# Kernel tuning notes

Hardware: AMD Instinct MI355X
Metric: run time of the kernel (lower is better)

## Reference

```python
import jax, jax.numpy as jnp
import numpy as np

V, D = 1_000_000, 128
N0, N1, N2 = 1_048_576, 131_072, 16_384
E0, E1, EP = 1_048_576, 131_072, 16_384


def setup_inputs() -> dict:
    key = jax.random.key(0)
    ks = jax.random.split(key, 20)
    inp = {
        'emb': jax.random.normal(ks[0], (V, D), jnp.float32) * 0.1,
        'bias': jnp.zeros((V, 1), jnp.float32),
        'nids': jax.random.randint(ks[1], (N0,), 0, V),
        'src0': jax.random.randint(ks[2], (E0,), 0, N0),
        'dst0': jax.random.randint(ks[3], (E0,), 0, N1),
        'w0': jax.random.uniform(ks[4], (E0,), jnp.float32),
        'src1': jax.random.randint(ks[5], (E1,), 0, N1),
        'dst1': jax.random.randint(ks[6], (E1,), 0, N2),
        'w1': jax.random.uniform(ks[7], (E1,), jnp.float32),
        'pos_src': jax.random.randint(ks[8], (EP,), 0, N2),
        'pos_dst': jax.random.randint(ks[9], (EP,), 0, N2),
        'neg_src': jax.random.randint(ks[10], (EP,), 0, N2),
        'neg_dst': jax.random.randint(ks[11], (EP,), 0, N2),
        'Q0w': jax.random.normal(ks[12], (D, D), jnp.float32) / np.sqrt(D),
        'Q0b': jnp.zeros((D,), jnp.float32),
        'W0w': jax.random.normal(ks[13], (2 * D, D), jnp.float32) / np.sqrt(2 * D),
        'W0b': jnp.zeros((D,), jnp.float32),
        'Q1w': jax.random.normal(ks[14], (D, D), jnp.float32) / np.sqrt(D),
        'Q1b': jnp.zeros((D,), jnp.float32),
        'W1w': jax.random.normal(ks[15], (2 * D, D), jnp.float32) / np.sqrt(2 * D),
        'W1b': jnp.zeros((D,), jnp.float32),
    }
    return inp


def _sage_conv(h_src, h_dst, src, dst, w, Qw, Qb, Ww, Wb, n_dst):
    # n = relu(Q h_src); m = sum_e w_e * n[src_e] per dst; ws = sum_e w_e per dst
    n = jax.nn.relu(h_src @ Qw + Qb)                                   # [N_src, H]
    m = jax.ops.segment_sum(n[src] * w[:, None], dst, num_segments=n_dst)
    ws = jnp.clip(jax.ops.segment_sum(w, dst, num_segments=n_dst), 1.0, None)[:, None]
    z = jax.nn.relu(jnp.concatenate([m / ws, h_dst], axis=1) @ Ww + Wb)
    zn = jnp.linalg.norm(z, axis=1, keepdims=True)
    return z / jnp.where(zn == 0, 1.0, zn)


def _pair_score(h, bias_nid, src, dst):
    # u_dot_v + bias_src + bias_dst  -> [E, 1]
    s = jnp.sum(h[src] * h[dst], axis=1, keepdims=True)
    return s + bias_nid[src] + bias_nid[dst]


def reference(emb, bias, nids, src0, dst0, w0, src1, dst1, w1,
              pos_src, pos_dst, neg_src, neg_dst,
              Q0w, Q0b, W0w, W0b, Q1w, Q1b, W1w, W1b):
    h = emb[nids]                                                      # [N0, D]
    h1 = _sage_conv(h, h[:N1], src0, dst0, w0, Q0w, Q0b, W0w, W0b, N1)  # [N1, D]
    h2 = _sage_conv(h1, h1[:N2], src1, dst1, w1, Q1w, Q1b, W1w, W1b, N2)  # [N2, D]
    h_item = emb[nids[:N2]] + h2                                       # [N2, D]
    bias_nid = bias[nids[:N2]]                                         # [N2, 1]
    pos = _pair_score(h_item, bias_nid, pos_src, pos_dst)
    neg = _pair_score(h_item, bias_nid, neg_src, neg_dst)
    return jax.nn.relu(neg - pos + 1.0)                                # [EP, 1]
```

## Files before the change

kernel.cpp:

```cpp
#include <hip/hip_runtime.h>
#include <stdint.h>

#define V_SZ   1000000
#define N0_SZ  1048576
#define N1_SZ  131072
#define N2_SZ  16384
#define E0_SZ  1048576
#define E1_SZ  131072
#define EP_SZ  16384

typedef short bf16x8 __attribute__((ext_vector_type(8)));
typedef float f32x4  __attribute__((ext_vector_type(4)));

__device__ __forceinline__ unsigned short f2bf(float f) {
  union { float f; unsigned u; } v; v.f = f;
  unsigned r = v.u + 0x7FFFu + ((v.u >> 16) & 1u);
  return (unsigned short)(r >> 16);
}
__device__ __forceinline__ float bf2f(unsigned short h) {
  union { unsigned u; float f; } v; v.u = ((unsigned)h) << 16;
  return v.f;
}
__device__ __forceinline__ unsigned pack2bf(float a, float b) {
  return ((unsigned)f2bf(b) << 16) | (unsigned)f2bf(a);
}

__global__ __launch_bounds__(256) void prepw_all_k(
    const float* __restrict__ Q0w, const float* __restrict__ W0w,
    const float* __restrict__ Q1w, const float* __restrict__ W1w,
    unsigned short* __restrict__ Q0T, unsigned short* __restrict__ W0T,
    unsigned short* __restrict__ Q1T, unsigned short* __restrict__ W1T) {
  int t = blockIdx.x * 256 + threadIdx.x;
  const float* W; unsigned short* WT; int K; int base;
  if (t < 16384)      { W = Q0w; WT = Q0T; K = 128; base = 0; }
  else if (t < 49152) { W = W0w; WT = W0T; K = 256; base = 16384; }
  else if (t < 65536) { W = Q1w; WT = Q1T; K = 128; base = 49152; }
  else                { W = W1w; WT = W1T; K = 256; base = 65536; }
  int u = t - base;
  int n = u & 127, k = u >> 7;
  WT[(size_t)n * K + k] = f2bf(W[u]);
}

__global__ __launch_bounds__(256) void hist_all_k(const int* __restrict__ dst0,
                                                  const int* __restrict__ dst1,
                                                  int* __restrict__ counts) {
  int e = blockIdx.x * 256 + threadIdx.x;
  if (e < E0_SZ) atomicAdd(&counts[dst0[e]], 1);
  else if (e < E0_SZ + E1_SZ) atomicAdd(&counts[N1_SZ + dst1[e - E0_SZ]], 1);
}

__global__ __launch_bounds__(256) void scan_bsums_k(const int* __restrict__ counts,
                                                    int* __restrict__ bsums) {
  __shared__ int red[256];
  int base = blockIdx.x * 1024, t = threadIdx.x;
  int s = 0;
  #pragma unroll
  for (int i = 0; i < 4; i++) s += counts[base + t * 4 + i];
  red[t] = s;
  __syncthreads();
  for (int st = 128; st > 0; st >>= 1) {
    if (t < st) red[t] += red[t + st];
    __syncthreads();
  }
  if (t == 0) bsums[blockIdx.x] = red[0];
}

__global__ __launch_bounds__(256) void scan_top2_k(int* __restrict__ bsums,
                                                   int* __restrict__ offs0_last,
                                                   int* __restrict__ offs1_last) {
  __shared__ int lds[256];
  int b = blockIdx.x, t = threadIdx.x;
  int nb = (b == 0) ? 128 : 16;
  int off = (b == 0) ? 0 : 128;
  int v = (t < nb) ? bsums[off + t] : 0;
  lds[t] = v;
  __syncthreads();
  for (int st = 1; st < 256; st <<= 1) {
    int x = (t >= st) ? lds[t - st] : 0;
    __syncthreads();
    lds[t] += x;
    __syncthreads();
  }
  if (t < nb) bsums[off + t] = lds[t] - v;
  if (t == nb - 1) *((b == 0) ? offs0_last : offs1_last) = lds[t];
}

__global__ __launch_bounds__(256) void scan_final_k(const int* __restrict__ counts,
                                                    const int* __restrict__ bsums,
                                                    int* __restrict__ offs0,
                                                    int* __restrict__ offs1) {
  __shared__ int tsum[256];
  int b = blockIdx.x, t = threadIdx.x;
  int base = b * 1024;
  int v0 = counts[base + t * 4 + 0], v1 = counts[base + t * 4 + 1];
  int v2 = counts[base + t * 4 + 2], v3 = counts[base + t * 4 + 3];
  int s = v0 + v1 + v2 + v3;
  tsum[t] = s;
  __syncthreads();
  for (int st = 1; st < 256; st <<= 1) {
    int x = (t >= st) ? tsum[t - st] : 0;
    __syncthreads();
    tsum[t] += x;
    __syncthreads();
  }
  int pre = bsums[b] + tsum[t] - s;
  int* op = (b < 128) ? (offs0 + base) : (offs1 + base - N1_SZ);
  op[t * 4 + 0] = pre;
  op[t * 4 + 1] = pre + v0;
  op[t * 4 + 2] = pre + v0 + v1;
  op[t * 4 + 3] = pre + v0 + v1 + v2;
}

__global__ __launch_bounds__(256) void scatter_all_k(
    const int* __restrict__ src0, const int* __restrict__ dst0, const float* __restrict__ w0,
    const int* __restrict__ src1, const int* __restrict__ dst1, const float* __restrict__ w1,
    const int* __restrict__ offs0, const int* __restrict__ offs1,
    int* __restrict__ cursor,
    int* __restrict__ srcs_s0, float* __restrict__ ws_s0,
    int* __restrict__ srcs_s1, float* __restrict__ ws_s1) {
  int e = blockIdx.x * 256 + threadIdx.x;
  if (e < E0_SZ) {
    int d = dst0[e];
    int p = offs0[d] + atomicAdd(&cursor[d], 1);
    srcs_s0[p] = src0[e];
    ws_s0[p] = w0[e];
  } else if (e < E0_SZ + E1_SZ) {
    int ee = e - E0_SZ;
    int d = dst1[ee];
    int p = offs1[d] + atomicAdd(&cursor[N1_SZ + d], 1);
    srcs_s1[p] = src1[ee];
    ws_s1[p] = w1[ee];
  }
}

#define AM_GATHER 0
#define AM_BF16   1
#define EPI_BF16        0
#define EPI_NORM        1
#define EPI_NORM_ADDEMB 2

template <int KCHUNKS, int AM0, int AM1, int EPI>
__global__ __launch_bounds__(256) void gemm_k(const void* __restrict__ asrc0,
                                              const void* __restrict__ asrc1,
                                              const int* __restrict__ ids,
                                              const unsigned short* __restrict__ BT,
                                              const float* __restrict__ biasv,
                                              void* __restrict__ outp,
                                              const float* __restrict__ emb) {
  __shared__ unsigned short lA[64][136];
  __shared__ unsigned short lB[128][136];
  const int tid = threadIdx.x;
  const int lane = tid & 63;
  const int wid = tid >> 6;
  const int rowbase = blockIdx.x * 64;
  const int Ktot = KCHUNKS * 128;

  f32x4 acc[8];
  #pragma unroll
  for (int i = 0; i < 8; i++) acc[i] = (f32x4){0.f, 0.f, 0.f, 0.f};

  for (int c = 0; c < KCHUNKS; ++c) {
    if (c) __syncthreads();
    const int am = (c == 0) ? AM0 : AM1;
    const void* asrc = (c == 0) ? asrc0 : asrc1;
    if (am == AM_GATHER) {
      const float* fsrc = (const float*)asrc;
      #pragma unroll
      for (int i = 0; i < 8; i++) {
        int f = i * 256 + tid;
        int r = f >> 5, c4 = f & 31;
        const float* rp = fsrc + (size_t)ids[rowbase + r] * 128;
        float4 v = *(const float4*)(rp + c4 * 4);
        uint2 pk;
        pk.x = pack2bf(v.x, v.y);
        pk.y = pack2bf(v.z, v.w);
        *(uint2*)(&lA[r][c4 * 4]) = pk;
      }
    } else {
      const unsigned short* bsrc = (const unsigned short*)asrc;
      #pragma unroll
      for (int i = 0; i < 4; i++) {
        int f = i * 256 + tid;
        int r = f >> 4, c8 = f & 15;
        uint4 v = *(const uint4*)(bsrc + (size_t)(rowbase + r) * 128 + c8 * 8);
        *(uint4*)(&lA[r][c8 * 8]) = v;
      }
    }
    {
      const unsigned short* bp = BT + c * 128;
      #pragma unroll
      for (int i = 0; i < 8; i++) {
        int f = i * 256 + tid;
        int n = f >> 4, c8 = f & 15;
        uint4 v = *(const uint4*)(bp + (size_t)n * Ktot + c8 * 8);
        *(uint4*)(&lB[n][c8 * 8]) = v;
      }
    }
    __syncthreads();

    const int mr = wid * 16 + (lane & 15);
    const int kq = (lane >> 4) * 8;
    #pragma unroll
    for (int kk = 0; kk < 128; kk += 32) {
      bf16x8 af = *(const bf16x8*)(&lA[mr][kk + kq]);
      #pragma unroll
      for (int nt = 0; nt < 8; ++nt) {
        bf16x8 bfr = *(const bf16x8*)(&lB[nt * 16 + (lane & 15)][kk + kq]);
        acc[nt] = __builtin_amdgcn_mfma_f32_16x16x32_bf16(af, bfr, acc[nt], 0, 0, 0);
      }
    }
  }

  const int crow = wid * 16 + ((lane >> 4) << 2);
  float vreg[8][4];
  #pragma unroll
  for (int nt = 0; nt < 8; ++nt) {
    int col = nt * 16 + (lane & 15);
    float b = biasv[col];
    #pragma unroll
    for (int r = 0; r < 4; ++r) {
      float v = acc[nt][r] + b;
      vreg[nt][r] = v > 0.f ? v : 0.f;
    }
  }
  if (EPI == EPI_BF16) {
    unsigned short* op = (unsigned short*)outp;
    #pragma unroll
    for (int nt = 0; nt < 8; ++nt) {
      int col = nt * 16 + (lane & 15);
      #pragma unroll
      for (int r = 0; r < 4; ++r)
        op[(size_t)(rowbase + crow + r) * 128 + col] = f2bf(vreg[nt][r]);
    }
  } else {
    float ss[4] = {0.f, 0.f, 0.f, 0.f};
    #pragma unroll
    for (int nt = 0; nt < 8; ++nt)
      #pragma unroll
      for (int r = 0; r < 4; ++r) ss[r] += vreg[nt][r] * vreg[nt][r];
    #pragma unroll
    for (int r = 0; r < 4; ++r) {
      ss[r] += __shfl_xor(ss[r], 1);
      ss[r] += __shfl_xor(ss[r], 2);
      ss[r] += __shfl_xor(ss[r], 4);
      ss[r] += __shfl_xor(ss[r], 8);
    }
    float sc[4];
    #pragma unroll
    for (int r = 0; r < 4; ++r) sc[r] = ss[r] > 0.f ? rsqrtf(ss[r]) : 1.0f;
    if (EPI == EPI_NORM) {
      unsigned short* op = (unsigned short*)outp;
      #pragma unroll
      for (int nt = 0; nt < 8; ++nt) {
        int col = nt * 16 + (lane & 15);
        #pragma unroll
        for (int r = 0; r < 4; ++r)
          op[(size_t)(rowbase + crow + r) * 128 + col] = f2bf(vreg[nt][r] * sc[r]);
      }
    } else {
      float* op = (float*)outp;
      #pragma unroll
      for (int nt = 0; nt < 8; ++nt) {
        int col = nt * 16 + (lane & 15);
        #pragma unroll
        for (int r = 0; r < 4; ++r) {
          int row = rowbase + crow + r;
          op[(size_t)row * 128 + col] =
              vreg[nt][r] * sc[r] + emb[(size_t)ids[row] * 128 + col];
        }
      }
    }
  }
}

__global__ __launch_bounds__(256) void agg_k(const unsigned short* __restrict__ nsrc,
                                             const int* __restrict__ offs,
                                             const int* __restrict__ srcs_s,
                                             const float* __restrict__ ws_s,
                                             unsigned short* __restrict__ aout, int ndst) {
  int wid = threadIdx.x >> 6, lane = threadIdx.x & 63;
  int d = blockIdx.x * 4 + wid;
  if (d >= ndst) return;
  int beg = offs[d], end = offs[d + 1];
  float ax = 0.f, ay = 0.f, wsum = 0.f;
  for (int base = beg; base < end; base += 64) {
    int cnt = min(64, end - base);
    int sv = 0; float wv = 0.f;
    if (lane < cnt) { sv = srcs_s[base + lane]; wv = ws_s[base + lane]; }
    int j = 0;
    for (; j + 4 <= cnt; j += 4) {
      int s0 = __shfl(sv, j),     s1 = __shfl(sv, j + 1);
      int s2 = __shfl(sv, j + 2), s3 = __shfl(sv, j + 3);
      float w0 = __shfl(wv, j),     w1 = __shfl(wv, j + 1);
      float w2 = __shfl(wv, j + 2), w3 = __shfl(wv, j + 3);
      unsigned u0 = *(const unsigned*)(nsrc + (size_t)s0 * 128 + lane * 2);
      unsigned u1 = *(const unsigned*)(nsrc + (size_t)s1 * 128 + lane * 2);
      unsigned u2 = *(const unsigned*)(nsrc + (size_t)s2 * 128 + lane * 2);
      unsigned u3 = *(const unsigned*)(nsrc + (size_t)s3 * 128 + lane * 2);
      ax += w0 * bf2f((unsigned short)(u0 & 0xffff));
      ay += w0 * bf2f((unsigned short)(u0 >> 16));
      ax += w1 * bf2f((unsigned short)(u1 & 0xffff));
      ay += w1 * bf2f((unsigned short)(u1 >> 16));
      ax += w2 * bf2f((unsigned short)(u2 & 0xffff));
      ay += w2 * bf2f((unsigned short)(u2 >> 16));
      ax += w3 * bf2f((unsigned short)(u3 & 0xffff));
      ay += w3 * bf2f((unsigned short)(u3 >> 16));
      wsum += w0 + w1 + w2 + w3;
    }
    for (; j < cnt; ++j) {
      int s = __shfl(sv, j);
      float w = __shfl(wv, j);
      unsigned u = *(const unsigned*)(nsrc + (size_t)s * 128 + lane * 2);
      ax += w * bf2f((unsigned short)(u & 0xffff));
      ay += w * bf2f((unsigned short)(u >> 16));
      wsum += w;
    }
  }
  float inv = 1.0f / fmaxf(wsum, 1.0f);
  unsigned o = ((unsigned)f2bf(ay * inv) << 16) | (unsigned)f2bf(ax * inv);
  *(unsigned*)(aout + (size_t)d * 128 + lane * 2) = o;
}

__global__ __launch_bounds__(256) void score_k(const float* __restrict__ hitem,
                                               const float* __restrict__ bias,
                                               const int* __restrict__ nids,
                                               const int* __restrict__ ps,
                                               const int* __restrict__ pd,
                                               const int* __restrict__ ns,
                                               const int* __restrict__ nd,
                                               float* __restrict__ out) {
  int wid = threadIdx.x >> 6, lane = threadIdx.x & 63;
  int e = blockIdx.x * 4 + wid;
  if (e >= EP_SZ) return;
  int a = ps[e], b = pd[e], c = ns[e], d = nd[e];
  float2 va = ((const float2*)(hitem + (size_t)a * 128))[lane];
  float2 vb = ((const float2*)(hitem + (size_t)b * 128))[lane];
  float2 vc = ((const float2*)(hitem + (size_t)c * 128))[lane];
  float2 vd = ((const float2*)(hitem + (size_t)d * 128))[lane];
  float dp = va.x * vb.x + va.y * vb.y;
  float dn = vc.x * vd.x + vc.y * vd.y;
  #pragma unroll
  for (int m = 1; m < 64; m <<= 1) {
    dp += __shfl_xor(dp, m);
    dn += __shfl_xor(dn, m);
  }
  if (lane == 0) {
    float sp = dp + bias[nids[a]] + bias[nids[b]];
    float sn = dn + bias[nids[c]] + bias[nids[d]];
    out[e] = fmaxf(sn - sp + 1.0f, 0.0f);
  }
}

extern "C" void kernel_launch(void* const* d_in, const int* in_sizes, int n_in,
                              void* d_out, int out_size, void* d_ws, size_t ws_size,
                              hipStream_t stream) {
  const float* emb  = (const float*)d_in[0];
  const float* bias = (const float*)d_in[1];
  const int* nids   = (const int*)d_in[2];
  const int* src0   = (const int*)d_in[3];
  const int* dst0   = (const int*)d_in[4];
  const float* w0   = (const float*)d_in[5];
  const int* src1   = (const int*)d_in[6];
  const int* dst1   = (const int*)d_in[7];
  const float* w1   = (const float*)d_in[8];
  const int* pos_src = (const int*)d_in[9];
  const int* pos_dst = (const int*)d_in[10];
  const int* neg_src = (const int*)d_in[11];
  const int* neg_dst = (const int*)d_in[12];
  const float* Q0w = (const float*)d_in[13];
  const float* Q0b = (const float*)d_in[14];
  const float* W0w = (const float*)d_in[15];
  const float* W0b = (const float*)d_in[16];
  const float* Q1w = (const float*)d_in[17];
  const float* Q1b = (const float*)d_in[18];
  const float* W1w = (const float*)d_in[19];
  const float* W1b = (const float*)d_in[20];
  float* out = (float*)d_out;

  char* ws = (char*)d_ws;
  size_t p = 0;
  auto carve = [&](size_t sz) { void* r = ws + p; p = (p + sz + 255) & ~(size_t)255; return r; };

  unsigned short* n0 = (unsigned short*)carve((size_t)N0_SZ * 128 * 2);
  unsigned short* h1    = (unsigned short*)(ws + 0);
  unsigned short* n1    = (unsigned short*)(ws + 33554432);
  unsigned short* a1    = (unsigned short*)(ws + 67108864);
  float*          hitem = (float*)(ws + 71303168);

  unsigned short* a0  = (unsigned short*)carve((size_t)N1_SZ * 128 * 2);
  unsigned short* Q0T = (unsigned short*)carve(128 * 128 * 2);
  unsigned short* W0T = (unsigned short*)carve(256 * 128 * 2);
  unsigned short* Q1T = (unsigned short*)carve(128 * 128 * 2);
  unsigned short* W1T = (unsigned short*)carve(256 * 128 * 2);
  int* cnt_all = (int*)carve((size_t)(N1_SZ + N2_SZ) * 2 * 4);
  int* counts  = cnt_all;
  int* cursor  = cnt_all + (N1_SZ + N2_SZ);
  int*   offs0   = (int*)carve((N1_SZ + 1) * 4);
  int*   offs1   = (int*)carve((N2_SZ + 1) * 4);
  int*   srcs_s0 = (int*)carve(E0_SZ * 4);
  float* ws_s0   = (float*)carve(E0_SZ * 4);
  int*   srcs_s1 = (int*)carve(E1_SZ * 4);
  float* ws_s1   = (float*)carve(E1_SZ * 4);
  int*   bsums   = (int*)carve(160 * 4);
  (void)ws_size; (void)in_sizes; (void)n_in; (void)out_size;

  hipMemsetAsync(cnt_all, 0, (size_t)(N1_SZ + N2_SZ) * 2 * 4, stream);

  prepw_all_k<<<384, 256, 0, stream>>>(Q0w, W0w, Q1w, W1w, Q0T, W0T, Q1T, W1T);

  hist_all_k<<<(E0_SZ + E1_SZ) / 256, 256, 0, stream>>>(dst0, dst1, counts);
  scan_bsums_k<<<(N1_SZ + N2_SZ) / 1024, 256, 0, stream>>>(counts, bsums);
  scan_top2_k<<<2, 256, 0, stream>>>(bsums, offs0 + N1_SZ, offs1 + N2_SZ);
  scan_final_k<<<(N1_SZ + N2_SZ) / 1024, 256, 0, stream>>>(counts, bsums, offs0, offs1);
  scatter_all_k<<<(E0_SZ + E1_SZ) / 256, 256, 0, stream>>>(
      src0, dst0, w0, src1, dst1, w1, offs0, offs1, cursor,
      srcs_s0, ws_s0, srcs_s1, ws_s1);

  gemm_k<1, AM_GATHER, AM_GATHER, EPI_BF16>
      <<<N0_SZ / 64, 256, 0, stream>>>(emb, nullptr, nids, Q0T, Q0b, n0, nullptr);
  agg_k<<<N1_SZ / 4, 256, 0, stream>>>(n0, offs0, srcs_s0, ws_s0, a0, N1_SZ);
  gemm_k<2, AM_BF16, AM_GATHER, EPI_NORM>
      <<<N1_SZ / 64, 256, 0, stream>>>(a0, emb, nids, W0T, W0b, h1, nullptr);
  gemm_k<1, AM_BF16, AM_BF16, EPI_BF16>
      <<<N1_SZ / 64, 256, 0, stream>>>(h1, nullptr, nullptr, Q1T, Q1b, n1, nullptr);
  agg_k<<<N2_SZ / 4, 256, 0, stream>>>(n1, offs1, srcs_s1, ws_s1, a1, N2_SZ);
  gemm_k<2, AM_BF16, AM_BF16, EPI_NORM_ADDEMB>
      <<<N2_SZ / 64, 256, 0, stream>>>(a1, h1, nids, W1T, W1b, hitem, emb);

  score_k<<<EP_SZ / 4, 256, 0, stream>>>(hitem, bias, nids, pos_src, pos_dst,
                                         neg_src, neg_dst, out);
}
```

Baseline: 1.041 ms.

## Fuse Q projection with edge aggregation by computing per-edge GEMM in dst-sorted order

Replaces the node-wise Q GEMM plus separate aggregation kernel with a per-edge GEMM over edges sorted by destination. Each block gathers its source rows, applies Q and ReLU, then segment-reduces within the block, writing complete destinations directly and partial sums for destinations straddling block boundaries. A fixup kernel combines those partials. Weight sums are now accumulated by atomics in the histogram kernel. This avoids materialising the full N0 x D intermediate but computes the GEMM per edge, duplicating work when a source appears in several edges, and adds atomics and a serial per-column reduction loop.

```diff
diff --git a/kernel.cpp b/kernel.cpp
--- a/kernel.cpp
+++ b/kernel.cpp
@@ -42,11 +42,22 @@
 }
 
 __global__ __launch_bounds__(256) void hist_all_k(const int* __restrict__ dst0,
+                                                  const float* __restrict__ w0,
                                                   const int* __restrict__ dst1,
-                                                  int* __restrict__ counts) {
+                                                  const float* __restrict__ w1,
+                                                  int* __restrict__ counts,
+                                                  float* __restrict__ wsumf) {
   int e = blockIdx.x * 256 + threadIdx.x;
-  if (e < E0_SZ) atomicAdd(&counts[dst0[e]], 1);
-  else if (e < E0_SZ + E1_SZ) atomicAdd(&counts[N1_SZ + dst1[e - E0_SZ]], 1);
+  if (e < E0_SZ) {
+    int d = dst0[e];
+    atomicAdd(&counts[d], 1);
+    atomicAdd(&wsumf[d], w0[e]);
+  } else if (e < E0_SZ + E1_SZ) {
+    int ee = e - E0_SZ;
+    int d = N1_SZ + dst1[ee];
+    atomicAdd(&counts[d], 1);
+    atomicAdd(&wsumf[d], w1[ee]);
+  }
 }
 
 __global__ __launch_bounds__(256) void scan_bsums_k(const int* __restrict__ counts,
@@ -114,28 +125,30 @@
 __global__ __launch_bounds__(256) void scatter_all_k(
     const int* __restrict__ src0, const int* __restrict__ dst0, const float* __restrict__ w0,
     const int* __restrict__ src1, const int* __restrict__ dst1, const float* __restrict__ w1,
+    const int* __restrict__ nids,
     const int* __restrict__ offs0, const int* __restrict__ offs1,
     int* __restrict__ cursor,
-    int* __restrict__ srcs_s0, float* __restrict__ ws_s0,
-    int* __restrict__ srcs_s1, float* __restrict__ ws_s1) {
+    int* __restrict__ gid0, float* __restrict__ ws_s0, int* __restrict__ edst0,
+    int* __restrict__ gid1, float* __restrict__ ws_s1, int* __restrict__ edst1) {
   int e = blockIdx.x * 256 + threadIdx.x;
   if (e < E0_SZ) {
     int d = dst0[e];
     int p = offs0[d] + atomicAdd(&cursor[d], 1);
-    srcs_s0[p] = src0[e];
+    gid0[p] = nids[src0[e]];
     ws_s0[p] = w0[e];
+    edst0[p] = d;
   } else if (e < E0_SZ + E1_SZ) {
     int ee = e - E0_SZ;
     int d = dst1[ee];
     int p = offs1[d] + atomicAdd(&cursor[N1_SZ + d], 1);
-    srcs_s1[p] = src1[ee];
+    gid1[p] = src1[ee];
     ws_s1[p] = w1[ee];
+    edst1[p] = d;
   }
 }
 
 #define AM_GATHER 0
 #define AM_BF16   1
-#define EPI_BF16        0
 #define EPI_NORM        1
 #define EPI_NORM_ADDEMB 2
 
@@ -223,101 +236,197 @@
       vreg[nt][r] = v > 0.f ? v : 0.f;
     }
   }
-  if (EPI == EPI_BF16) {
+  float ss[4] = {0.f, 0.f, 0.f, 0.f};
+  #pragma unroll
+  for (int nt = 0; nt < 8; ++nt)
+    #pragma unroll
+    for (int r = 0; r < 4; ++r) ss[r] += vreg[nt][r] * vreg[nt][r];
+  #pragma unroll
+  for (int r = 0; r < 4; ++r) {
+    ss[r] += __shfl_xor(ss[r], 1);
+    ss[r] += __shfl_xor(ss[r], 2);
+    ss[r] += __shfl_xor(ss[r], 4);
+    ss[r] += __shfl_xor(ss[r], 8);
+  }
+  float sc[4];
+  #pragma unroll
+  for (int r = 0; r < 4; ++r) sc[r] = ss[r] > 0.f ? rsqrtf(ss[r]) : 1.0f;
+  if (EPI == EPI_NORM) {
     unsigned short* op = (unsigned short*)outp;
     #pragma unroll
     for (int nt = 0; nt < 8; ++nt) {
       int col = nt * 16 + (lane & 15);
       #pragma unroll
       for (int r = 0; r < 4; ++r)
-        op[(size_t)(rowbase + crow + r) * 128 + col] = f2bf(vreg[nt][r]);
+        op[(size_t)(rowbase + crow + r) * 128 + col] = f2bf(vreg[nt][r] * sc[r]);
     }
   } else {
-    float ss[4] = {0.f, 0.f, 0.f, 0.f};
-    #pragma unroll
-    for (int nt = 0; nt < 8; ++nt)
+    float* op = (float*)outp;
+    #pragma unroll
+    for (int nt = 0; nt < 8; ++nt) {
+      int col = nt * 16 + (lane & 15);
       #pragma unroll
-      for (int r = 0; r < 4; ++r) ss[r] += vreg[nt][r] * vreg[nt][r];
+      for (int r = 0; r < 4; ++r) {
+        int row = rowbase + crow + r;
+        op[(size_t)row * 128 + col] =
+            vreg[nt][r] * sc[r] + emb[(size_t)ids[row] * 128 + col];
+      }
+    }
+  }
+}
+
+template <int AMODE>
+__global__ __launch_bounds__(256) void gemm_agg_k(
+    const void* __restrict__ asrc, const int* __restrict__ gids,
+    const int* __restrict__ edge_dst, const float* __restrict__ ws_s,
+    const int* __restrict__ offs, const float* __restrict__ wsum,
+    const unsigned short* __restrict__ BT, const float* __restrict__ biasv,
+    unsigned short* __restrict__ aout, float* __restrict__ partial) {
+  __shared__ __align__(16) char smem[52224];
+  unsigned short (*lA)[136] = (unsigned short(*)[136])smem;
+  unsigned short (*lB)[136] = (unsigned short(*)[136])(smem + 17408);
+  float (*scr)[132] = (float(*)[132])smem;
+  __shared__ int dstL[64];
+  __shared__ float wL[64];
+  __shared__ int offsL[65];
+  __shared__ float wsumL[64];
+
+  const int tid = threadIdx.x;
+  const int lane = tid & 63;
+  const int wid = tid >> 6;
+  const int rowbase = blockIdx.x * 64;
+
+  if (tid < 64) {
+    dstL[tid] = edge_dst[rowbase + tid];
+    wL[tid] = ws_s[rowbase + tid];
+  }
+
+  if (AMODE == 0) {
+    const float* fsrc = (const float*)asrc;
+    #pragma unroll
+    for (int i = 0; i < 8; i++) {
+      int f = i * 256 + tid;
+      int r = f >> 5, c4 = f & 31;
+      const float* rp = fsrc + (size_t)gids[rowbase + r] * 128;
+      float4 v = *(const float4*)(rp + c4 * 4);
+      uint2 pk;
+      pk.x = pack2bf(v.x, v.y);
+      pk.y = pack2bf(v.z, v.w);
+      *(uint2*)(&lA[r][c4 * 4]) = pk;
+    }
+  } else {
+    const unsigned short* bsrc = (const unsigned short*)asrc;
+    #pragma unroll
+    for (int i = 0; i < 4; i++) {
+      int f = i * 256 + tid;
+      int r = f >> 4, c8 = f & 15;
+      uint4 v = *(const uint4*)(bsrc + (size_t)gids[rowbase + r] * 128 + c8 * 8);
+      *(uint4*)(&lA[r][c8 * 8]) = v;
+    }
+  }
+  #pragma unroll
+  for (int i = 0; i < 8; i++) {
+    int f = i * 256 + tid;
+    int n = f >> 4, c8 = f & 15;
+    uint4 v = *(const uint4*)(BT + (size_t)n * 128 + c8 * 8);
+    *(uint4*)(&lB[n][c8 * 8]) = v;
+  }
+  __syncthreads();
+
+  const int first = dstL[0];
+  const int nd = dstL[63] - first + 1;
+  if (tid < nd + 1) offsL[tid] = offs[first + tid];
+  if (tid < nd) wsumL[tid] = wsum[first + tid];
+
+  f32x4 acc[8];
+  #pragma unroll
+  for (int i = 0; i < 8; i++) acc[i] = (f32x4){0.f, 0.f, 0.f, 0.f};
+  const int mr = wid * 16 + (lane & 15);
+  const int kq = (lane >> 4) * 8;
+  #pragma unroll
+  for (int kk = 0; kk < 128; kk += 32) {
+    bf16x8 af = *(const bf16x8*)(&lA[mr][kk + kq]);
+    #pragma unroll
+    for (int nt = 0; nt < 8; ++nt) {
+      bf16x8 bfr = *(const bf16x8*)(&lB[nt * 16 + (lane & 15)][kk + kq]);
+      acc[nt] = __builtin_amdgcn_mfma_f32_16x16x32_bf16(af, bfr, acc[nt], 0, 0, 0);
+    }
+  }
+
+  const int crow = wid * 16 + ((lane >> 4) << 2);
+  float vreg[8][4];
+  #pragma unroll
+  for (int nt = 0; nt < 8; ++nt) {
+    int col = nt * 16 + (lane & 15);
+    float b = biasv[col];
     #pragma unroll
     for (int r = 0; r < 4; ++r) {
-      ss[r] += __shfl_xor(ss[r], 1);
-      ss[r] += __shfl_xor(ss[r], 2);
-      ss[r] += __shfl_xor(ss[r], 4);
-      ss[r] += __shfl_xor(ss[r], 8);
-    }
-    float sc[4];
-    #pragma unroll
-    for (int r = 0; r < 4; ++r) sc[r] = ss[r] > 0.f ? rsqrtf(ss[r]) : 1.0f;
-    if (EPI == EPI_NORM) {
-      unsigned short* op = (unsigned short*)outp;
-      #pragma unroll
-      for (int nt = 0; nt < 8; ++nt) {
-        int col = nt * 16 + (lane & 15);
-        #pragma unroll
-        for (int r = 0; r < 4; ++r)
-          op[(size_t)(rowbase + crow + r) * 128 + col] = f2bf(vreg[nt][r] * sc[r]);
-      }
-    } else {
-      float* op = (float*)outp;
-      #pragma unroll
-      for (int nt = 0; nt < 8; ++nt) {
-        int col = nt * 16 + (lane & 15);
-        #pragma unroll
-        for (int r = 0; r < 4; ++r) {
-          int row = rowbase + crow + r;
-          op[(size_t)row * 128 + col] =
-              vreg[nt][r] * sc[r] + emb[(size_t)ids[row] * 128 + col];
-        }
-      }
-    }
-  }
-}
-
-__global__ __launch_bounds__(256) void agg_k(const unsigned short* __restrict__ nsrc,
-                                             const int* __restrict__ offs,
-                                             const int* __restrict__ srcs_s,
-                                             const float* __restrict__ ws_s,
-                                             unsigned short* __restrict__ aout, int ndst) {
+      float v = acc[nt][r] + b;
+      vreg[nt][r] = v > 0.f ? v : 0.f;
+    }
+  }
+  __syncthreads();
+  #pragma unroll
+  for (int nt = 0; nt < 8; ++nt) {
+    int col = nt * 16 + (lane & 15);
+    #pragma unroll
+    for (int r = 0; r < 4; ++r) scr[crow + r][col] = vreg[nt][r];
+  }
+  __syncthreads();
+
+  if (tid < 128) {
+    const int col = tid;
+    auto flush = [&](int d, float a) {
+      int di = d - first;
+      if (offsL[di] >= rowbase && offsL[di + 1] <= rowbase + 64) {
+        float inv = 1.0f / fmaxf(wsumL[di], 1.0f);
+        aout[(size_t)d * 128 + col] = f2bf(a * inv);
+      } else {
+        int slot = (d == first) ? 0 : 1;
+        partial[(((size_t)blockIdx.x << 1) + slot) * 128 + col] = a;
+      }
+    };
+    float a = 0.f;
+    int cur = first;
+    for (int r = 0; r < 64; ++r) {
+      int d = dstL[r];
+      if (d != cur) {
+        flush(cur, a);
+        a = 0.f;
+        cur = d;
+      }
+      a += scr[r][col] * wL[r];
+    }
+    flush(cur, a);
+  }
+}
+
+__global__ __launch_bounds__(256) void fixup_k(const int* __restrict__ offs,
+                                               const int* __restrict__ edge_dst,
+                                               const float* __restrict__ wsum,
+                                               const float* __restrict__ partial,
+                                               unsigned short* __restrict__ aout,
+                                               int ndst) {
   int wid = threadIdx.x >> 6, lane = threadIdx.x & 63;
   int d = blockIdx.x * 4 + wid;
   if (d >= ndst) return;
   int beg = offs[d], end = offs[d + 1];
-  float ax = 0.f, ay = 0.f, wsum = 0.f;
-  for (int base = beg; base < end; base += 64) {
-    int cnt = min(64, end - base);
-    int sv = 0; float wv = 0.f;
-    if (lane < cnt) { sv = srcs_s[base + lane]; wv = ws_s[base + lane]; }
-    int j = 0;
-    for (; j + 4 <= cnt; j += 4) {
-      int s0 = __shfl(sv, j),     s1 = __shfl(sv, j + 1);
-      int s2 = __shfl(sv, j + 2), s3 = __shfl(sv, j + 3);
-      float w0 = __shfl(wv, j),     w1 = __shfl(wv, j + 1);
-      float w2 = __shfl(wv, j + 2), w3 = __shfl(wv, j + 3);
-      unsigned u0 = *(const unsigned*)(nsrc + (size_t)s0 * 128 + lane * 2);
-      unsigned u1 = *(const unsigned*)(nsrc + (size_t)s1 * 128 + lane * 2);
-      unsigned u2 = *(const unsigned*)(nsrc + (size_t)s2 * 128 + lane * 2);
-      unsigned u3 = *(const unsigned*)(nsrc + (size_t)s3 * 128 + lane * 2);
-      ax += w0 * bf2f((unsigned short)(u0 & 0xffff));
-      ay += w0 * bf2f((unsigned short)(u0 >> 16));
-      ax += w1 * bf2f((unsigned short)(u1 & 0xffff));
-      ay += w1 * bf2f((unsigned short)(u1 >> 16));
-      ax += w2 * bf2f((unsigned short)(u2 & 0xffff));
-      ay += w2 * bf2f((unsigned short)(u2 >> 16));
-      ax += w3 * bf2f((unsigned short)(u3 & 0xffff));
-      ay += w3 * bf2f((unsigned short)(u3 >> 16));
-      wsum += w0 + w1 + w2 + w3;
-    }
-    for (; j < cnt; ++j) {
-      int s = __shfl(sv, j);
-      float w = __shfl(wv, j);
-      unsigned u = *(const unsigned*)(nsrc + (size_t)s * 128 + lane * 2);
-      ax += w * bf2f((unsigned short)(u & 0xffff));
-      ay += w * bf2f((unsigned short)(u >> 16));
-      wsum += w;
-    }
-  }
-  float inv = 1.0f / fmaxf(wsum, 1.0f);
-  unsigned o = ((unsigned)f2bf(ay * inv) << 16) | (unsigned)f2bf(ax * inv);
+  if (beg == end) {
+    *(unsigned*)(aout + (size_t)d * 128 + lane * 2) = 0u;
+    return;
+  }
+  int b0 = beg >> 6, b1 = (end - 1) >> 6;
+  if (b0 == b1) return;
+  float s0 = 0.f, s1 = 0.f;
+  for (int b = b0; b <= b1; ++b) {
+    int fd = edge_dst[b * 64];
+    int slot = (d == fd) ? 0 : 1;
+    float2 v = *(const float2*)(partial + (((size_t)b << 1) + slot) * 128 + lane * 2);
+    s0 += v.x;
+    s1 += v.y;
+  }
+  float inv = 1.0f / fmaxf(wsum[d], 1.0f);
+  unsigned o = ((unsigned)f2bf(s1 * inv) << 16) | (unsigned)f2bf(s0 * inv);
   *(unsigned*)(aout + (size_t)d * 128 + lane * 2) = o;
 }
 
@@ -381,49 +490,56 @@
   size_t p = 0;
   auto carve = [&](size_t sz) { void* r = ws + p; p = (p + sz + 255) & ~(size_t)255; return r; };
 
-  unsigned short* n0 = (unsigned short*)carve((size_t)N0_SZ * 128 * 2);
-  unsigned short* h1    = (unsigned short*)(ws + 0);
-  unsigned short* n1    = (unsigned short*)(ws + 33554432);
-  unsigned short* a1    = (unsigned short*)(ws + 67108864);
-  float*          hitem = (float*)(ws + 71303168);
-
-  unsigned short* a0  = (unsigned short*)carve((size_t)N1_SZ * 128 * 2);
+  unsigned short* a0    = (unsigned short*)carve((size_t)N1_SZ * 128 * 2);
+  unsigned short* h1    = (unsigned short*)carve((size_t)N1_SZ * 128 * 2);
+  unsigned short* a1    = (unsigned short*)carve((size_t)N2_SZ * 128 * 2);
+  float*          hitem = (float*)carve((size_t)N2_SZ * 128 * 4);
   unsigned short* Q0T = (unsigned short*)carve(128 * 128 * 2);
   unsigned short* W0T = (unsigned short*)carve(256 * 128 * 2);
   unsigned short* Q1T = (unsigned short*)carve(128 * 128 * 2);
   unsigned short* W1T = (unsigned short*)carve(256 * 128 * 2);
-  int* cnt_all = (int*)carve((size_t)(N1_SZ + N2_SZ) * 2 * 4);
-  int* counts  = cnt_all;
-  int* cursor  = cnt_all + (N1_SZ + N2_SZ);
-  int*   offs0   = (int*)carve((N1_SZ + 1) * 4);
-  int*   offs1   = (int*)carve((N2_SZ + 1) * 4);
-  int*   srcs_s0 = (int*)carve(E0_SZ * 4);
-  float* ws_s0   = (float*)carve(E0_SZ * 4);
-  int*   srcs_s1 = (int*)carve(E1_SZ * 4);
-  float* ws_s1   = (float*)carve(E1_SZ * 4);
-  int*   bsums   = (int*)carve(160 * 4);
+  int* cnt_all = (int*)carve((size_t)(N1_SZ + N2_SZ) * 3 * 4);
+  int*   counts = cnt_all;
+  int*   cursor = cnt_all + (N1_SZ + N2_SZ);
+  float* wsumf  = (float*)(cnt_all + 2 * (N1_SZ + N2_SZ));
+  float* wsum0 = wsumf;
+  float* wsum1 = wsumf + N1_SZ;
+  int*   offs0 = (int*)carve((N1_SZ + 1) * 4);
+  int*   offs1 = (int*)carve((N2_SZ + 1) * 4);
+  int*   gid0  = (int*)carve(E0_SZ * 4);
+  float* ws_s0 = (float*)carve(E0_SZ * 4);
+  int*   edst0 = (int*)carve(E0_SZ * 4);
+  int*   gid1  = (int*)carve(E1_SZ * 4);
+  float* ws_s1 = (float*)carve(E1_SZ * 4);
+  int*   edst1 = (int*)carve(E1_SZ * 4);
+  float* partial0 = (float*)carve((size_t)(E0_SZ / 64) * 2 * 128 * 4);
+  float* partial1 = (float*)carve((size_t)(E1_SZ / 64) * 2 * 128 * 4);
+  int*   bsums = (int*)carve(160 * 4);
   (void)ws_size; (void)in_sizes; (void)n_in; (void)out_size;
 
-  hipMemsetAsync(cnt_all, 0, (size_t)(N1_SZ + N2_SZ) * 2 * 4, stream);
+  hipMemsetAsync(cnt_all, 0, (size_t)(N1_SZ + N2_SZ) * 3 * 4, stream);
 
   prepw_all_k<<<384, 256, 0, stream>>>(Q0w, W0w, Q1w, W1w, Q0T, W0T, Q1T, W1T);
 
-  hist_all_k<<<(E0_SZ + E1_SZ) / 256, 256, 0, stream>>>(dst0, dst1, counts);
+  hist_all_k<<<(E0_SZ + E1_SZ) / 256, 256, 0, stream>>>(dst0, w0, dst1, w1, counts, wsumf);
   scan_bsums_k<<<(N1_SZ + N2_SZ) / 1024, 256, 0, stream>>>(counts, bsums);
   scan_top2_k<<<2, 256, 0, stream>>>(bsums, offs0 + N1_SZ, offs1 + N2_SZ);
   scan_final_k<<<(N1_SZ + N2_SZ) / 1024, 256, 0, stream>>>(counts, bsums, offs0, offs1);
   scatter_all_k<<<(E0_SZ + E1_SZ) / 256, 256, 0, stream>>>(
-      src0, dst0, w0, src1, dst1, w1, offs0, offs1, cursor,
-      srcs_s0, ws_s0, srcs_s1, ws_s1);
-
-  gemm_k<1, AM_GATHER, AM_GATHER, EPI_BF16>
-      <<<N0_SZ / 64, 256, 0, stream>>>(emb, nullptr, nids, Q0T, Q0b, n0, nullptr);
-  agg_k<<<N1_SZ / 4, 256, 0, stream>>>(n0, offs0, srcs_s0, ws_s0, a0, N1_SZ);
+      src0, dst0, w0, src1, dst1, w1, nids, offs0, offs1, cursor,
+      gid0, ws_s0, edst0, gid1, ws_s1, edst1);
+
+  gemm_agg_k<0><<<E0_SZ / 64, 256, 0, stream>>>(emb, gid0, edst0, ws_s0, offs0,
+                                                wsum0, Q0T, Q0b, a0, partial0);
+  fixup_k<<<N1_SZ / 4, 256, 0, stream>>>(offs0, edst0, wsum0, partial0, a0, N1_SZ);
+
   gemm_k<2, AM_BF16, AM_GATHER, EPI_NORM>
       <<<N1_SZ / 64, 256, 0, stream>>>(a0, emb, nids, W0T, W0b, h1, nullptr);
-  gemm_k<1, AM_BF16, AM_BF16, EPI_BF16>
-      <<<N1_SZ / 64, 256, 0, stream>>>(h1, nullptr, nullptr, Q1T, Q1b, n1, nullptr);
-  agg_k<<<N2_SZ / 4, 256, 0, stream>>>(n1, offs1, srcs_s1, ws_s1, a1, N2_SZ);
+
+  gemm_agg_k<1><<<E1_SZ / 64, 256, 0, stream>>>(h1, gid1, edst1, ws_s1, offs1,
+                                                wsum1, Q1T, Q1b, a1, partial1);
+  fixup_k<<<N2_SZ / 4, 256, 0, stream>>>(offs1, edst1, wsum1, partial1, a1, N2_SZ);
+
   gemm_k<2, AM_BF16, AM_BF16, EPI_NORM_ADDEMB>
       <<<N2_SZ / 64, 256, 0, stream>>>(a1, h1, nids, W1T, W1b, hitem, emb);
 
```

Result: slower. 1.151 ms (+10.6%).
